# Kernel tuning notes

Measured on AMD Instinct MI355X. Metric: run time of the kernel, lower is better.

The kernel has to match this reference:

```python
import jax, jax.numpy as jnp
import numpy as np

N, F = 100000, 64   # input (up) nodes, feature dim
M, K = 100000, 32   # down nodes, neighbors per node


def setup_inputs() -> dict:
    key = jax.random.key(0)
    k1, k2, k3, k4 = jax.random.split(key, 4)
    features = jax.random.normal(k1, (N, F), dtype=jnp.float32)
    sel_idx_up = jax.random.randint(k2, (N, 1), 0, M, dtype=jnp.int64)
    weights_down = jax.random.uniform(k3, (M, K, 1), dtype=jnp.float32)
    nidx_down = jax.random.randint(k4, (M, K), 0, M, dtype=jnp.int64)
    return {
        "features": features,
        "weights_down": weights_down,
        "sel_idx_up": sel_idx_up,
        "nidx_down": nidx_down,
    }


def reference(features, weights_down, sel_idx_up, nidx_down):
    # PullDown, mode='mean', weights=None.
    m = weights_down.shape[0]
    f_dim = features.shape[1]
    # tf.scatter_nd: duplicate indices accumulate (add)
    down_f = jnp.zeros((m, f_dim), dtype=features.dtype).at[sel_idx_up[:, 0]].add(features)
    # acc_knn weighted mean over K neighbors; nidx == -1 means invalid (zero contribution)
    mask = nidx_down >= 0                              # [M, K]
    idx = jnp.where(mask, nidx_down, 0)
    gathered = down_f[idx] * weights_down              # [M, K, F]
    gathered = jnp.where(mask[..., None], gathered, jnp.zeros((), dtype=features.dtype))
    out = jnp.mean(gathered, axis=1)                   # divide by K, as acc_sum's *K implies
    return out.reshape(-1, f_dim)
```

## Files before the change

kernel.cpp:

```cpp
#include <hip/hip_runtime.h>
#include <hip/hip_bf16.h>

#define F_DIM 64
#define K_NB  32
#define CAP   16

typedef float        f32x4 __attribute__((ext_vector_type(4)));
typedef int          i32x4 __attribute__((ext_vector_type(4)));
typedef unsigned int u32;

__device__ inline u32 f2b(float f) {
    u32 u = __float_as_uint(f);
    u32 r = ((u >> 16) & 1u) + 0x7fffu;
    return (u + r) >> 16;
}
__device__ inline float blo(u32 u) { return __uint_as_float(u << 16); }
__device__ inline float bhi(u32 u) { return __uint_as_float(u & 0xffff0000u); }

__global__ __launch_bounds__(256) void bucket_fill_kernel(
    const int* __restrict__ sel_idx,
    int*       __restrict__ cnt,
    int*       __restrict__ bucket,
    int N)
{
    int i = blockIdx.x * blockDim.x + threadIdx.x;
    if (i >= N) return;
    int m = sel_idx[i];
    int slot = atomicAdd(&cnt[m], 1);
    if (slot < CAP) bucket[m * CAP + slot] = i;
}

__global__ __launch_bounds__(256) void build_down_f_bf16_kernel(
    const f32x4* __restrict__ features4,
    const int*   __restrict__ cnt,
    const int*   __restrict__ bucket,
    unsigned short* __restrict__ down_h,
    int M)
{
    int t = blockIdx.x * blockDim.x + threadIdx.x;
    int m = t >> 4;
    int q = t & 15;
    if (m >= M) return;
    int c = cnt[m]; c = c < CAP ? c : CAP;
    const int* bk = bucket + m * CAP;

    int b0 = bk[0], b1 = bk[1], b2 = bk[2], b3 = bk[3];
    int i0 = (0 < c) ? b0 : 0;  float g0 = (0 < c) ? 1.f : 0.f;
    int i1 = (1 < c) ? b1 : 0;  float g1 = (1 < c) ? 1.f : 0.f;
    int i2 = (2 < c) ? b2 : 0;  float g2 = (2 < c) ? 1.f : 0.f;
    int i3 = (3 < c) ? b3 : 0;  float g3 = (3 < c) ? 1.f : 0.f;

    f32x4 v0 = features4[(size_t)i0 * 16 + q];
    f32x4 v1 = features4[(size_t)i1 * 16 + q];
    f32x4 v2 = features4[(size_t)i2 * 16 + q];
    f32x4 v3 = features4[(size_t)i3 * 16 + q];

    f32x4 acc;
    acc.x = g0 * v0.x + g1 * v1.x + g2 * v2.x + g3 * v3.x;
    acc.y = g0 * v0.y + g1 * v1.y + g2 * v2.y + g3 * v3.y;
    acc.z = g0 * v0.z + g1 * v1.z + g2 * v2.z + g3 * v3.z;
    acc.w = g0 * v0.w + g1 * v1.w + g2 * v2.w + g3 * v3.w;

    if (c > 4) {
        for (int j = 4; j < c; ++j) {
            int i = bk[j];
            f32x4 v = features4[(size_t)i * 16 + q];
            acc.x += v.x; acc.y += v.y; acc.z += v.z; acc.w += v.w;
        }
    }
    uint2 o;
    o.x = f2b(acc.x) | (f2b(acc.y) << 16);
    o.y = f2b(acc.z) | (f2b(acc.w) << 16);
    *(uint2*)(down_h + (size_t)m * F_DIM + q * 4) = o;
}

__global__ __launch_bounds__(256) void gather_mean_bf16_kernel(
    const unsigned short* __restrict__ down_h,
    const f32x4*          __restrict__ weights4,
    const i32x4*          __restrict__ nidx4,
    f32x4*                __restrict__ out4,
    int M)
{
    int t = blockIdx.x * blockDim.x + threadIdx.x;
    int m = t >> 3;
    int q = t & 7;
    if (m >= M) return;

    const i32x4* ni = nidx4    + (size_t)m * (K_NB / 4);
    const f32x4* wp = weights4 + (size_t)m * (K_NB / 4);
    const uint4* base = (const uint4*)down_h + q;

    float a0 = 0.f, a1 = 0.f, a2 = 0.f, a3 = 0.f;
    float a4 = 0.f, a5 = 0.f, a6 = 0.f, a7 = 0.f;

    #pragma unroll
    for (int b = 0; b < 4; ++b) {
        i32x4 I0 = ni[2 * b], I1 = ni[2 * b + 1];
        f32x4 W0 = wp[2 * b], W1 = wp[2 * b + 1];
        int j0 = I0.x < 0 ? 0 : I0.x;  float w0 = I0.x < 0 ? 0.f : W0.x;
        int j1 = I0.y < 0 ? 0 : I0.y;  float w1 = I0.y < 0 ? 0.f : W0.y;
        int j2 = I0.z < 0 ? 0 : I0.z;  float w2 = I0.z < 0 ? 0.f : W0.z;
        int j3 = I0.w < 0 ? 0 : I0.w;  float w3 = I0.w < 0 ? 0.f : W0.w;
        int j4 = I1.x < 0 ? 0 : I1.x;  float w4 = I1.x < 0 ? 0.f : W1.x;
        int j5 = I1.y < 0 ? 0 : I1.y;  float w5 = I1.y < 0 ? 0.f : W1.y;
        int j6 = I1.z < 0 ? 0 : I1.z;  float w6 = I1.z < 0 ? 0.f : W1.z;
        int j7 = I1.w < 0 ? 0 : I1.w;  float w7 = I1.w < 0 ? 0.f : W1.w;

        uint4 g0 = base[(size_t)j0 * 8];
        uint4 g1 = base[(size_t)j1 * 8];
        uint4 g2 = base[(size_t)j2 * 8];
        uint4 g3 = base[(size_t)j3 * 8];
        uint4 g4 = base[(size_t)j4 * 8];
        uint4 g5 = base[(size_t)j5 * 8];
        uint4 g6 = base[(size_t)j6 * 8];
        uint4 g7 = base[(size_t)j7 * 8];

        a0 += w0 * blo(g0.x); a1 += w0 * bhi(g0.x); a2 += w0 * blo(g0.y); a3 += w0 * bhi(g0.y);
        a4 += w0 * blo(g0.z); a5 += w0 * bhi(g0.z); a6 += w0 * blo(g0.w); a7 += w0 * bhi(g0.w);
        a0 += w1 * blo(g1.x); a1 += w1 * bhi(g1.x); a2 += w1 * blo(g1.y); a3 += w1 * bhi(g1.y);
        a4 += w1 * blo(g1.z); a5 += w1 * bhi(g1.z); a6 += w1 * blo(g1.w); a7 += w1 * bhi(g1.w);
        a0 += w2 * blo(g2.x); a1 += w2 * bhi(g2.x); a2 += w2 * blo(g2.y); a3 += w2 * bhi(g2.y);
        a4 += w2 * blo(g2.z); a5 += w2 * bhi(g2.z); a6 += w2 * blo(g2.w); a7 += w2 * bhi(g2.w);
        a0 += w3 * blo(g3.x); a1 += w3 * bhi(g3.x); a2 += w3 * blo(g3.y); a3 += w3 * bhi(g3.y);
        a4 += w3 * blo(g3.z); a5 += w3 * bhi(g3.z); a6 += w3 * blo(g3.w); a7 += w3 * bhi(g3.w);
        a0 += w4 * blo(g4.x); a1 += w4 * bhi(g4.x); a2 += w4 * blo(g4.y); a3 += w4 * bhi(g4.y);
        a4 += w4 * blo(g4.z); a5 += w4 * bhi(g4.z); a6 += w4 * blo(g4.w); a7 += w4 * bhi(g4.w);
        a0 += w5 * blo(g5.x); a1 += w5 * bhi(g5.x); a2 += w5 * blo(g5.y); a3 += w5 * bhi(g5.y);
        a4 += w5 * blo(g5.z); a5 += w5 * bhi(g5.z); a6 += w5 * blo(g5.w); a7 += w5 * bhi(g5.w);
        a0 += w6 * blo(g6.x); a1 += w6 * bhi(g6.x); a2 += w6 * blo(g6.y); a3 += w6 * bhi(g6.y);
        a4 += w6 * blo(g6.z); a5 += w6 * bhi(g6.z); a6 += w6 * blo(g6.w); a7 += w6 * bhi(g6.w);
        a0 += w7 * blo(g7.x); a1 += w7 * bhi(g7.x); a2 += w7 * blo(g7.y); a3 += w7 * bhi(g7.y);
        a4 += w7 * blo(g7.z); a5 += w7 * bhi(g7.z); a6 += w7 * blo(g7.w); a7 += w7 * bhi(g7.w);
    }

    const float s = 1.0f / (float)K_NB;
    size_t o = (size_t)m * 16 + q * 2;
    f32x4 r0; r0.x = a0 * s; r0.y = a1 * s; r0.z = a2 * s; r0.w = a3 * s;
    f32x4 r1; r1.x = a4 * s; r1.y = a5 * s; r1.z = a6 * s; r1.w = a7 * s;
    out4[o + 0] = r0;
    out4[o + 1] = r1;
}

__global__ __launch_bounds__(256) void scatter_add_kernel(
    const float* __restrict__ features, const int* __restrict__ sel_idx,
    float* __restrict__ down_f, int N)
{
    int t = blockIdx.x * blockDim.x + threadIdx.x;
    int i  = t >> 5;
    int fp = (t & 31);
    if (i >= N) return;
    int dst = sel_idx[i];
    float2 v = ((const float2*)features)[(size_t)i * (F_DIM / 2) + fp];
    float* d = down_f + (size_t)dst * F_DIM + fp * 2;
    atomicAdd(d + 0, v.x);
    atomicAdd(d + 1, v.y);
}

__global__ __launch_bounds__(256) void gather_mean_f32_kernel(
    const float2* __restrict__ down_f2, const float* __restrict__ weights,
    const int* __restrict__ nidx, float2* __restrict__ out2, int M)
{
    int t  = blockIdx.x * blockDim.x + threadIdx.x;
    int m  = t >> 5;
    int fp = t & 31;
    if (m >= M) return;
    const i32x4* ni4 = (const i32x4*)(nidx    + (size_t)m * K_NB);
    const f32x4* wp4 = (const f32x4*)(weights + (size_t)m * K_NB);
    float accx = 0.f, accy = 0.f;
    #pragma unroll
    for (int q = 0; q < K_NB / 4; ++q) {
        i32x4 iv = ni4[q];
        f32x4 wv = wp4[q];
        int i0 = iv.x < 0 ? 0 : iv.x;  float w0 = iv.x < 0 ? 0.f : wv.x;
        int i1 = iv.y < 0 ? 0 : iv.y;  float w1 = iv.y < 0 ? 0.f : wv.y;
        int i2 = iv.z < 0 ? 0 : iv.z;  float w2 = iv.z < 0 ? 0.f : wv.z;
        int i3 = iv.w < 0 ? 0 : iv.w;  float w3 = iv.w < 0 ? 0.f : wv.w;
        float2 v0 = down_f2[(size_t)i0 * (F_DIM / 2) + fp];
        float2 v1 = down_f2[(size_t)i1 * (F_DIM / 2) + fp];
        float2 v2 = down_f2[(size_t)i2 * (F_DIM / 2) + fp];
        float2 v3 = down_f2[(size_t)i3 * (F_DIM / 2) + fp];
        accx += w0 * v0.x; accy += w0 * v0.y;
        accx += w1 * v1.x; accy += w1 * v1.y;
        accx += w2 * v2.x; accy += w2 * v2.y;
        accx += w3 * v3.x; accy += w3 * v3.y;
    }
    float2 r;
    r.x = accx * (1.0f / (float)K_NB);
    r.y = accy * (1.0f / (float)K_NB);
    out2[(size_t)m * (F_DIM / 2) + fp] = r;
}

extern "C" void kernel_launch(void* const* d_in, const int* in_sizes, int n_in,
                              void* d_out, int out_size, void* d_ws, size_t ws_size,
                              hipStream_t stream) {
    const float* features = (const float*)d_in[0];
    const float* weights  = (const float*)d_in[1];
    const int*   sel_idx  = (const int*)  d_in[2];
    const int*   nidx     = (const int*)  d_in[3];
    float*       out      = (float*)d_out;

    const int N = in_sizes[2];
    const int M = in_sizes[3] / K_NB;

    size_t downh_bytes  = (size_t)M * F_DIM * sizeof(unsigned short);
    size_t cnt_bytes    = (size_t)M * sizeof(int);
    size_t bucket_bytes = (size_t)M * CAP * sizeof(int);

    if (ws_size >= downh_bytes + cnt_bytes + bucket_bytes) {
        unsigned short* down_h = (unsigned short*)d_ws;
        int* cnt    = (int*)((char*)d_ws + downh_bytes);
        int* bucket = cnt + M;

        hipMemsetAsync(cnt, 0, cnt_bytes, stream);
        bucket_fill_kernel<<<(N + 255) / 256, 256, 0, stream>>>(
            sel_idx, cnt, bucket, N);
        build_down_f_bf16_kernel<<<(M * 16 + 255) / 256, 256, 0, stream>>>(
            (const f32x4*)features, cnt, bucket, down_h, M);
        gather_mean_bf16_kernel<<<(M * 8 + 255) / 256, 256, 0, stream>>>(
            down_h, (const f32x4*)weights, (const i32x4*)nidx,
            (f32x4*)out, M);
    } else {
        float* down_f = (float*)d_ws;
        hipMemsetAsync(down_f, 0, (size_t)M * F_DIM * sizeof(float), stream);
        scatter_add_kernel<<<(N * 32 + 255) / 256, 256, 0, stream>>>(
            features, sel_idx, down_f, N);
        gather_mean_f32_kernel<<<(M * 32 + 255) / 256, 256, 0, stream>>>(
            (const float2*)down_f, weights, nidx, (float2*)out, M);
    }
}
```

Before: 156.0 us.

## Fuse pulldown stages into one cooperative kernel with compacted bf16 table

Replaces the memset plus three kernel launches with a single cooperative persistent kernel that uses grid-wide syncs between the stages. Only occupied down nodes are stored, in a compacted bf16 table, and the neighbour indices are rewritten as packed 16-bit slot ids. Invalid or empty neighbours point to a zero row, so the per-neighbour mask selects are no longer needed. The aims are to cut launch overhead, shrink the gather working set to raise cache hits, and halve index traffic. The cost is four grid syncs and an extra remap pass, and the 16-bit packing only holds while the number of occupied nodes stays below 65536.

```diff
diff --git a/kernel.cpp b/kernel.cpp
--- a/kernel.cpp
+++ b/kernel.cpp
@@ -1,12 +1,18 @@
 #include <hip/hip_runtime.h>
-#include <hip/hip_bf16.h>
+#include <hip/hip_cooperative_groups.h>
+
+namespace cg = cooperative_groups;
 
 #define F_DIM 64
 #define K_NB  32
 #define CAP   16
+#define GRID_BLOCKS 1024
+#define BLOCK       256
 
 typedef float        f32x4 __attribute__((ext_vector_type(4)));
 typedef int          i32x4 __attribute__((ext_vector_type(4)));
+typedef unsigned int u32x4 __attribute__((ext_vector_type(4)));
+typedef unsigned int u32x2 __attribute__((ext_vector_type(2)));
 typedef unsigned int u32;
 
 __device__ inline u32 f2b(float f) {
@@ -16,6 +22,161 @@
 }
 __device__ inline float blo(u32 u) { return __uint_as_float(u << 16); }
 __device__ inline float bhi(u32 u) { return __uint_as_float(u & 0xffff0000u); }
+
+__global__ __launch_bounds__(BLOCK, 4) void fused_pulldown_kernel(
+    const f32x4* __restrict__ features4,
+    const f32x4* __restrict__ weights4,
+    const i32x4* __restrict__ nidx4,
+    const int*   __restrict__ sel_idx,
+    f32x4*       __restrict__ out4,
+    unsigned short* __restrict__ down_h,
+    int*         __restrict__ bucket,
+    int*         __restrict__ cnt,
+    int*         __restrict__ nz,
+    int*         __restrict__ remap,
+    int N, int M)
+{
+    cg::grid_group grid = cg::this_grid();
+    const int tid0    = blockIdx.x * BLOCK + threadIdx.x;
+    const int gstride = gridDim.x * blockDim.x;
+
+    for (int i = tid0; i < M; i += gstride) { cnt[i] = 0; remap[i] = 0; }
+    if (tid0 == 0) *nz = 0;
+    if (tid0 < 16) { u32x2 z; z.x = 0u; z.y = 0u; ((u32x2*)down_h)[tid0] = z; }
+    grid.sync();
+
+    for (int i = tid0; i < N; i += gstride) {
+        int m = sel_idx[i];
+        int slot = atomicAdd(&cnt[m], 1);
+        if (slot < CAP) bucket[m * CAP + slot] = i;
+        if (slot == 0) remap[m] = 1 + atomicAdd(nz, 1);
+    }
+    grid.sync();
+
+    for (int t = tid0; t < M * 16; t += gstride) {
+        int m = t >> 4;
+        int q = t & 15;
+        int c = cnt[m];
+        if (c == 0) continue;
+        c = c < CAP ? c : CAP;
+        int s = remap[m];
+        const i32x4* b4p = (const i32x4*)(bucket + m * CAP);
+        i32x4 b4 = b4p[0];
+
+        int i0 = b4.x;
+        int i1 = (1 < c) ? b4.y : 0;  float g1 = (1 < c) ? 1.f : 0.f;
+        int i2 = (2 < c) ? b4.z : 0;  float g2 = (2 < c) ? 1.f : 0.f;
+        int i3 = (3 < c) ? b4.w : 0;  float g3 = (3 < c) ? 1.f : 0.f;
+
+        f32x4 v0 = __builtin_nontemporal_load(&features4[(size_t)i0 * 16 + q]);
+        f32x4 v1 = __builtin_nontemporal_load(&features4[(size_t)i1 * 16 + q]);
+        f32x4 v2 = __builtin_nontemporal_load(&features4[(size_t)i2 * 16 + q]);
+        f32x4 v3 = __builtin_nontemporal_load(&features4[(size_t)i3 * 16 + q]);
+
+        f32x4 acc;
+        acc.x = v0.x + g1 * v1.x + g2 * v2.x + g3 * v3.x;
+        acc.y = v0.y + g1 * v1.y + g2 * v2.y + g3 * v3.y;
+        acc.z = v0.z + g1 * v1.z + g2 * v2.z + g3 * v3.z;
+        acc.w = v0.w + g1 * v1.w + g2 * v2.w + g3 * v3.w;
+
+        if (c > 4) {
+            const int* bk = bucket + m * CAP;
+            for (int j = 4; j < c; ++j) {
+                int i = bk[j];
+                f32x4 v = __builtin_nontemporal_load(&features4[(size_t)i * 16 + q]);
+                acc.x += v.x; acc.y += v.y; acc.z += v.z; acc.w += v.w;
+            }
+        }
+        u32x2 o;
+        o.x = f2b(acc.x) | (f2b(acc.y) << 16);
+        o.y = f2b(acc.z) | (f2b(acc.w) << 16);
+        *(u32x2*)(down_h + (size_t)s * F_DIM + q * 4) = o;
+    }
+    grid.sync();
+
+    {
+        u32x4* nidx_c = (u32x4*)bucket;
+        const int TT = M * (K_NB / 8);
+        for (int t = tid0; t < TT; t += gstride) {
+            i32x4 I0 = __builtin_nontemporal_load(nidx4 + 2 * t);
+            i32x4 I1 = __builtin_nontemporal_load(nidx4 + 2 * t + 1);
+            u32 r0 = (u32)remap[I0.x < 0 ? 0 : I0.x];  r0 = I0.x < 0 ? 0u : r0;
+            u32 r1 = (u32)remap[I0.y < 0 ? 0 : I0.y];  r1 = I0.y < 0 ? 0u : r1;
+            u32 r2 = (u32)remap[I0.z < 0 ? 0 : I0.z];  r2 = I0.z < 0 ? 0u : r2;
+            u32 r3 = (u32)remap[I0.w < 0 ? 0 : I0.w];  r3 = I0.w < 0 ? 0u : r3;
+            u32 r4 = (u32)remap[I1.x < 0 ? 0 : I1.x];  r4 = I1.x < 0 ? 0u : r4;
+            u32 r5 = (u32)remap[I1.y < 0 ? 0 : I1.y];  r5 = I1.y < 0 ? 0u : r5;
+            u32 r6 = (u32)remap[I1.z < 0 ? 0 : I1.z];  r6 = I1.z < 0 ? 0u : r6;
+            u32 r7 = (u32)remap[I1.w < 0 ? 0 : I1.w];  r7 = I1.w < 0 ? 0u : r7;
+            u32x4 o;
+            o.x = r0 | (r1 << 16);
+            o.y = r2 | (r3 << 16);
+            o.z = r4 | (r5 << 16);
+            o.w = r6 | (r7 << 16);
+            __builtin_nontemporal_store(o, nidx_c + t);
+        }
+    }
+    grid.sync();
+
+    {
+        const u32x4* nidx_c = (const u32x4*)bucket;
+        for (int t = tid0; t < M * 8; t += gstride) {
+            int m = t >> 3;
+            int q = t & 7;
+            const u32x4* ncp = nidx_c + (size_t)m * 4;
+            const f32x4* wp  = weights4 + (size_t)m * (K_NB / 4);
+            const unsigned char* bp =
+                (const unsigned char*)down_h + (unsigned)q * 16u;
+
+            float a0 = 0.f, a1 = 0.f, a2 = 0.f, a3 = 0.f;
+            float a4 = 0.f, a5 = 0.f, a6 = 0.f, a7 = 0.f;
+
+            #pragma unroll
+            for (int b = 0; b < 4; ++b) {
+                u32x4 I  = __builtin_nontemporal_load(ncp + b);
+                f32x4 W0 = __builtin_nontemporal_load(wp + 2 * b);
+                f32x4 W1 = __builtin_nontemporal_load(wp + 2 * b + 1);
+                u32 r0 = I.x & 0xffffu, r1 = I.x >> 16;
+                u32 r2 = I.y & 0xffffu, r3 = I.y >> 16;
+                u32 r4 = I.z & 0xffffu, r5 = I.z >> 16;
+                u32 r6 = I.w & 0xffffu, r7 = I.w >> 16;
+
+                u32x4 g0 = *(const u32x4*)(bp + (size_t)(r0 * 128u));
+                u32x4 g1 = *(const u32x4*)(bp + (size_t)(r1 * 128u));
+                u32x4 g2 = *(const u32x4*)(bp + (size_t)(r2 * 128u));
+                u32x4 g3 = *(const u32x4*)(bp + (size_t)(r3 * 128u));
+                u32x4 g4 = *(const u32x4*)(bp + (size_t)(r4 * 128u));
+                u32x4 g5 = *(const u32x4*)(bp + (size_t)(r5 * 128u));
+                u32x4 g6 = *(const u32x4*)(bp + (size_t)(r6 * 128u));
+                u32x4 g7 = *(const u32x4*)(bp + (size_t)(r7 * 128u));
+
+                a0 += W0.x * blo(g0.x); a1 += W0.x * bhi(g0.x); a2 += W0.x * blo(g0.y); a3 += W0.x * bhi(g0.y);
+                a4 += W0.x * blo(g0.z); a5 += W0.x * bhi(g0.z); a6 += W0.x * blo(g0.w); a7 += W0.x * bhi(g0.w);
+                a0 += W0.y * blo(g1.x); a1 += W0.y * bhi(g1.x); a2 += W0.y * blo(g1.y); a3 += W0.y * bhi(g1.y);
+                a4 += W0.y * blo(g1.z); a5 += W0.y * bhi(g1.z); a6 += W0.y * blo(g1.w); a7 += W0.y * bhi(g1.w);
+                a0 += W0.z * blo(g2.x); a1 += W0.z * bhi(g2.x); a2 += W0.z * blo(g2.y); a3 += W0.z * bhi(g2.y);
+                a4 += W0.z * blo(g2.z); a5 += W0.z * bhi(g2.z); a6 += W0.z * blo(g2.w); a7 += W0.z * bhi(g2.w);
+                a0 += W0.w * blo(g3.x); a1 += W0.w * bhi(g3.x); a2 += W0.w * blo(g3.y); a3 += W0.w * bhi(g3.y);
+                a4 += W0.w * blo(g3.z); a5 += W0.w * bhi(g3.z); a6 += W0.w * blo(g3.w); a7 += W0.w * bhi(g3.w);
+                a0 += W1.x * blo(g4.x); a1 += W1.x * bhi(g4.x); a2 += W1.x * blo(g4.y); a3 += W1.x * bhi(g4.y);
+                a4 += W1.x * blo(g4.z); a5 += W1.x * bhi(g4.z); a6 += W1.x * blo(g4.w); a7 += W1.x * bhi(g4.w);
+                a0 += W1.y * blo(g5.x); a1 += W1.y * bhi(g5.x); a2 += W1.y * blo(g5.y); a3 += W1.y * bhi(g5.y);
+                a4 += W1.y * blo(g5.z); a5 += W1.y * bhi(g5.z); a6 += W1.y * blo(g5.w); a7 += W1.y * bhi(g5.w);
+                a0 += W1.z * blo(g6.x); a1 += W1.z * bhi(g6.x); a2 += W1.z * blo(g6.y); a3 += W1.z * bhi(g6.y);
+                a4 += W1.z * blo(g6.z); a5 += W1.z * bhi(g6.z); a6 += W1.z * blo(g6.w); a7 += W1.z * bhi(g6.w);
+                a0 += W1.w * blo(g7.x); a1 += W1.w * bhi(g7.x); a2 += W1.w * blo(g7.y); a3 += W1.w * bhi(g7.y);
+                a4 += W1.w * blo(g7.z); a5 += W1.w * bhi(g7.z); a6 += W1.w * blo(g7.w); a7 += W1.w * bhi(g7.w);
+            }
+
+            const float s = 1.0f / (float)K_NB;
+            size_t o = (size_t)m * 16 + q * 2;
+            f32x4 r0v; r0v.x = a0 * s; r0v.y = a1 * s; r0v.z = a2 * s; r0v.w = a3 * s;
+            f32x4 r1v; r1v.x = a4 * s; r1v.y = a5 * s; r1v.z = a6 * s; r1v.w = a7 * s;
+            __builtin_nontemporal_store(r0v, &out4[o + 0]);
+            __builtin_nontemporal_store(r1v, &out4[o + 1]);
+        }
+    }
+}
 
 __global__ __launch_bounds__(256) void bucket_fill_kernel(
     const int* __restrict__ sel_idx,
@@ -68,10 +229,10 @@
             acc.x += v.x; acc.y += v.y; acc.z += v.z; acc.w += v.w;
         }
     }
-    uint2 o;
+    u32x2 o;
     o.x = f2b(acc.x) | (f2b(acc.y) << 16);
     o.y = f2b(acc.z) | (f2b(acc.w) << 16);
-    *(uint2*)(down_h + (size_t)m * F_DIM + q * 4) = o;
+    *(u32x2*)(down_h + (size_t)m * F_DIM + q * 4) = o;
 }
 
 __global__ __launch_bounds__(256) void gather_mean_bf16_kernel(
@@ -88,7 +249,7 @@
 
     const i32x4* ni = nidx4    + (size_t)m * (K_NB / 4);
     const f32x4* wp = weights4 + (size_t)m * (K_NB / 4);
-    const uint4* base = (const uint4*)down_h + q;
+    const u32x4* base = (const u32x4*)down_h + q;
 
     float a0 = 0.f, a1 = 0.f, a2 = 0.f, a3 = 0.f;
     float a4 = 0.f, a5 = 0.f, a6 = 0.f, a7 = 0.f;
@@ -106,14 +267,14 @@
         int j6 = I1.z < 0 ? 0 : I1.z;  float w6 = I1.z < 0 ? 0.f : W1.z;
         int j7 = I1.w < 0 ? 0 : I1.w;  float w7 = I1.w < 0 ? 0.f : W1.w;
 
-        uint4 g0 = base[(size_t)j0 * 8];
-        uint4 g1 = base[(size_t)j1 * 8];
-        uint4 g2 = base[(size_t)j2 * 8];
-        uint4 g3 = base[(size_t)j3 * 8];
-        uint4 g4 = base[(size_t)j4 * 8];
-        uint4 g5 = base[(size_t)j5 * 8];
-        uint4 g6 = base[(size_t)j6 * 8];
-        uint4 g7 = base[(size_t)j7 * 8];
+        u32x4 g0 = base[(size_t)j0 * 8];
+        u32x4 g1 = base[(size_t)j1 * 8];
+        u32x4 g2 = base[(size_t)j2 * 8];
+        u32x4 g3 = base[(size_t)j3 * 8];
+        u32x4 g4 = base[(size_t)j4 * 8];
+        u32x4 g5 = base[(size_t)j5 * 8];
+        u32x4 g6 = base[(size_t)j6 * 8];
+        u32x4 g7 = base[(size_t)j7 * 8];
 
         a0 += w0 * blo(g0.x); a1 += w0 * bhi(g0.x); a2 += w0 * blo(g0.y); a3 += w0 * bhi(g0.y);
         a4 += w0 * blo(g0.z); a5 += w0 * bhi(g0.z); a6 += w0 * blo(g0.w); a7 += w0 * bhi(g0.w);
@@ -202,26 +363,79 @@
     const int N = in_sizes[2];
     const int M = in_sizes[3] / K_NB;
 
-    size_t downh_bytes  = (size_t)M * F_DIM * sizeof(unsigned short);
+    size_t downh_bytes  = (size_t)(M + 1) * F_DIM * sizeof(unsigned short);
+    size_t bucket_bytes = (size_t)M * CAP * sizeof(int);
     size_t cnt_bytes    = (size_t)M * sizeof(int);
-    size_t bucket_bytes = (size_t)M * CAP * sizeof(int);
-
-    if (ws_size >= downh_bytes + cnt_bytes + bucket_bytes) {
+    size_t nz_bytes     = 16;
+    size_t remap_bytes  = (size_t)M * sizeof(int);
+
+    if (ws_size >= downh_bytes + bucket_bytes + cnt_bytes + nz_bytes + remap_bytes) {
         unsigned short* down_h = (unsigned short*)d_ws;
-        int* cnt    = (int*)((char*)d_ws + downh_bytes);
-        int* bucket = cnt + M;
-
-        hipMemsetAsync(cnt, 0, cnt_bytes, stream);
-        bucket_fill_kernel<<<(N + 255) / 256, 256, 0, stream>>>(
-            sel_idx, cnt, bucket, N);
-        build_down_f_bf16_kernel<<<(M * 16 + 255) / 256, 256, 0, stream>>>(
-            (const f32x4*)features, cnt, bucket, down_h, M);
-        gather_mean_bf16_kernel<<<(M * 8 + 255) / 256, 256, 0, stream>>>(
-            down_h, (const f32x4*)weights, (const i32x4*)nidx,
-            (f32x4*)out, M);
+        int* bucket = (int*)((char*)d_ws + downh_bytes);
+        int* cnt    = (int*)((char*)d_ws + downh_bytes + bucket_bytes);
+        int* nz     = (int*)((char*)cnt + cnt_bytes);
+        int* remap  = (int*)((char*)nz + nz_bytes);
+
+        static int coop_state = 0;
+        static int coop_grid  = 0;
+        if (coop_state == 0 && coop_grid == 0) {
+            int maxB = 0, cus = 0, dev = 0;
+            (void)hipGetDevice(&dev);
+            if (hipOccupancyMaxActiveBlocksPerMultiprocessor(
+                    &maxB, (const void*)fused_pulldown_kernel, BLOCK, 0) == hipSuccess &&
+                hipDeviceGetAttribute(&cus, hipDeviceAttributeMultiprocessorCount,
+                                      dev) == hipSuccess &&
+                maxB > 0 && cus > 0) {
+                long cap = (long)maxB * (long)cus;
+                coop_grid = (int)(cap < GRID_BLOCKS ? cap : GRID_BLOCKS);
+            } else {
+                coop_state = -1;
+                coop_grid  = -1;
+            }
+        }
+
+        hipStreamCaptureStatus cap_st = hipStreamCaptureStatusNone;
+        (void)hipStreamIsCapturing(stream, &cap_st);
+        bool capturing = (cap_st != hipStreamCaptureStatusNone);
+        bool try_coop = (coop_state == 1) || (coop_state == 0 && !capturing);
+
+        bool done = false;
+        if (try_coop && coop_grid > 0) {
+            const f32x4* features4 = (const f32x4*)features;
+            const f32x4* weights4  = (const f32x4*)weights;
+            const i32x4* nidx4     = (const i32x4*)nidx;
+            f32x4*       out4      = (f32x4*)out;
+            int Nv = N, Mv = M;
+            void* args[] = {
+                (void*)&features4, (void*)&weights4, (void*)&nidx4,
+                (void*)&sel_idx,   (void*)&out4,     (void*)&down_h,
+                (void*)&bucket,    (void*)&cnt,      (void*)&nz,
+                (void*)&remap,     (void*)&Nv,       (void*)&Mv,
+            };
+            hipError_t err = hipLaunchCooperativeKernel(
+                (void*)fused_pulldown_kernel, dim3(coop_grid), dim3(BLOCK),
+                args, 0, stream);
+            if (err == hipSuccess) {
+                done = true;
+                if (coop_state == 0) coop_state = 1;
+            } else {
+                coop_state = -1;
+            }
+        }
+
+        if (!done) {
+            (void)hipMemsetAsync(cnt, 0, cnt_bytes, stream);
+            bucket_fill_kernel<<<(N + 255) / 256, 256, 0, stream>>>(
+                sel_idx, cnt, bucket, N);
+            build_down_f_bf16_kernel<<<(M * 16 + 255) / 256, 256, 0, stream>>>(
+                (const f32x4*)features, cnt, bucket, down_h, M);
+            gather_mean_bf16_kernel<<<(M * 8 + 255) / 256, 256, 0, stream>>>(
+                down_h, (const f32x4*)weights, (const i32x4*)nidx,
+                (f32x4*)out, M);
+        }
     } else {
         float* down_f = (float*)d_ws;
-        hipMemsetAsync(down_f, 0, (size_t)M * F_DIM * sizeof(float), stream);
+        (void)hipMemsetAsync(down_f, 0, (size_t)M * F_DIM * sizeof(float), stream);
         scatter_add_kernel<<<(N * 32 + 255) / 256, 256, 0, stream>>>(
             features, sel_idx, down_f, N);
         gather_mean_f32_kernel<<<(M * 32 + 255) / 256, 256, 0, stream>>>(
```

After: 436.2 us. 2.8x slower.

## Fuse three pulldown kernels into one persistent kernel with grid barriers

Applied to the files above, without the earlier changes.

Replaces the bucket-fill, bf16 build, and gather-mean launches with a single persistent grid-stride kernel. Stages are separated by software grid barriers built on atomic counters and flags kept in the workspace. The aim is to remove per-launch overhead and inter-kernel gaps. In exchange, the grid is capped by occupancy, spin-barriers add cost, and correctness relies on all blocks being co-resident.

```diff
diff --git a/kernel.cpp b/kernel.cpp
--- a/kernel.cpp
+++ b/kernel.cpp
@@ -1,12 +1,15 @@
 #include <hip/hip_runtime.h>
-#include <hip/hip_bf16.h>
 
 #define F_DIM 64
 #define K_NB  32
 #define CAP   16
+#define BLOCK 256
+#define MAX_GRID 2048
 
 typedef float        f32x4 __attribute__((ext_vector_type(4)));
 typedef int          i32x4 __attribute__((ext_vector_type(4)));
+typedef unsigned int u32x4 __attribute__((ext_vector_type(4)));
+typedef unsigned int u32x2 __attribute__((ext_vector_type(2)));
 typedef unsigned int u32;
 
 __device__ inline u32 f2b(float f) {
@@ -17,11 +20,149 @@
 __device__ inline float blo(u32 u) { return __uint_as_float(u << 16); }
 __device__ inline float bhi(u32 u) { return __uint_as_float(u & 0xffff0000u); }
 
+__device__ inline void grid_barrier(int* state, int idx, int nblocks) {
+    __syncthreads();
+    if (threadIdx.x == 0) {
+        int* arrive = state + idx * 64;
+        int* flag   = state + idx * 64 + 32;
+        __threadfence();
+        int prev = __hip_atomic_fetch_add(arrive, 1, __ATOMIC_ACQ_REL,
+                                          __HIP_MEMORY_SCOPE_AGENT);
+        if (prev == nblocks - 1) {
+            __hip_atomic_store(flag, 1, __ATOMIC_RELEASE,
+                               __HIP_MEMORY_SCOPE_AGENT);
+        } else {
+            while (__hip_atomic_load(flag, __ATOMIC_ACQUIRE,
+                                     __HIP_MEMORY_SCOPE_AGENT) == 0) {
+                __builtin_amdgcn_s_sleep(8);
+            }
+        }
+        __threadfence();
+    }
+    __syncthreads();
+}
+
+__global__ __launch_bounds__(BLOCK) void fused_pulldown_kernel(
+    const f32x4* __restrict__ features4,
+    const f32x4* __restrict__ weights4,
+    const i32x4* __restrict__ nidx4,
+    const int*   __restrict__ sel_idx,
+    f32x4*       __restrict__ out4,
+    unsigned short* __restrict__ down_h,
+    int*         __restrict__ bucket,
+    int*         __restrict__ cnt,
+    int*         __restrict__ bstate,
+    int N, int M, int nblocks)
+{
+    const int tid0    = blockIdx.x * BLOCK + threadIdx.x;
+    const int gstride = gridDim.x * BLOCK;
+
+    for (int i = tid0; i < N; i += gstride) {
+        int m = sel_idx[i];
+        int slot = atomicAdd(&cnt[m], 1);
+        if (slot < CAP) bucket[m * CAP + slot] = i;
+    }
+    grid_barrier(bstate, 0, nblocks);
+
+    for (int t = tid0; t < M * 16; t += gstride) {
+        int m = t >> 4;
+        int q = t & 15;
+        int c = cnt[m]; c = c < CAP ? c : CAP;
+        i32x4 b4 = *(const i32x4*)(bucket + m * CAP);
+
+        int i0 = (0 < c) ? b4.x : 0;  float g0 = (0 < c) ? 1.f : 0.f;
+        int i1 = (1 < c) ? b4.y : 0;  float g1 = (1 < c) ? 1.f : 0.f;
+        int i2 = (2 < c) ? b4.z : 0;  float g2 = (2 < c) ? 1.f : 0.f;
+        int i3 = (3 < c) ? b4.w : 0;  float g3 = (3 < c) ? 1.f : 0.f;
+
+        f32x4 v0 = features4[(size_t)i0 * 16 + q];
+        f32x4 v1 = features4[(size_t)i1 * 16 + q];
+        f32x4 v2 = features4[(size_t)i2 * 16 + q];
+        f32x4 v3 = features4[(size_t)i3 * 16 + q];
+
+        f32x4 acc;
+        acc.x = g0 * v0.x + g1 * v1.x + g2 * v2.x + g3 * v3.x;
+        acc.y = g0 * v0.y + g1 * v1.y + g2 * v2.y + g3 * v3.y;
+        acc.z = g0 * v0.z + g1 * v1.z + g2 * v2.z + g3 * v3.z;
+        acc.w = g0 * v0.w + g1 * v1.w + g2 * v2.w + g3 * v3.w;
+
+        if (c > 4) {
+            const int* bk = bucket + m * CAP;
+            for (int j = 4; j < c; ++j) {
+                int i = bk[j];
+                f32x4 v = features4[(size_t)i * 16 + q];
+                acc.x += v.x; acc.y += v.y; acc.z += v.z; acc.w += v.w;
+            }
+        }
+        u32x2 o;
+        o.x = f2b(acc.x) | (f2b(acc.y) << 16);
+        o.y = f2b(acc.z) | (f2b(acc.w) << 16);
+        *(u32x2*)(down_h + (size_t)m * F_DIM + q * 4) = o;
+    }
+    grid_barrier(bstate, 1, nblocks);
+
+    for (int t = tid0; t < M * 8; t += gstride) {
+        int m = t >> 3;
+        int q = t & 7;
+        const i32x4* ni = nidx4    + (size_t)m * (K_NB / 4);
+        const f32x4* wp = weights4 + (size_t)m * (K_NB / 4);
+        const u32x4* base = (const u32x4*)down_h + q;
+
+        float a0 = 0.f, a1 = 0.f, a2 = 0.f, a3 = 0.f;
+        float a4 = 0.f, a5 = 0.f, a6 = 0.f, a7 = 0.f;
+
+        #pragma unroll
+        for (int b = 0; b < 4; ++b) {
+            i32x4 I0 = ni[2 * b], I1 = ni[2 * b + 1];
+            f32x4 W0 = wp[2 * b], W1 = wp[2 * b + 1];
+            int j0 = I0.x < 0 ? 0 : I0.x;  float w0 = I0.x < 0 ? 0.f : W0.x;
+            int j1 = I0.y < 0 ? 0 : I0.y;  float w1 = I0.y < 0 ? 0.f : W0.y;
+            int j2 = I0.z < 0 ? 0 : I0.z;  float w2 = I0.z < 0 ? 0.f : W0.z;
+            int j3 = I0.w < 0 ? 0 : I0.w;  float w3 = I0.w < 0 ? 0.f : W0.w;
+            int j4 = I1.x < 0 ? 0 : I1.x;  float w4 = I1.x < 0 ? 0.f : W1.x;
+            int j5 = I1.y < 0 ? 0 : I1.y;  float w5 = I1.y < 0 ? 0.f : W1.y;
+            int j6 = I1.z < 0 ? 0 : I1.z;  float w6 = I1.z < 0 ? 0.f : W1.z;
+            int j7 = I1.w < 0 ? 0 : I1.w;  float w7 = I1.w < 0 ? 0.f : W1.w;
+
+            u32x4 g0 = base[(size_t)j0 * 8];
+            u32x4 g1 = base[(size_t)j1 * 8];
+            u32x4 g2 = base[(size_t)j2 * 8];
+            u32x4 g3 = base[(size_t)j3 * 8];
+            u32x4 g4 = base[(size_t)j4 * 8];
+            u32x4 g5 = base[(size_t)j5 * 8];
+            u32x4 g6 = base[(size_t)j6 * 8];
+            u32x4 g7 = base[(size_t)j7 * 8];
+
+            a0 += w0 * blo(g0.x); a1 += w0 * bhi(g0.x); a2 += w0 * blo(g0.y); a3 += w0 * bhi(g0.y);
+            a4 += w0 * blo(g0.z); a5 += w0 * bhi(g0.z); a6 += w0 * blo(g0.w); a7 += w0 * bhi(g0.w);
+            a0 += w1 * blo(g1.x); a1 += w1 * bhi(g1.x); a2 += w1 * blo(g1.y); a3 += w1 * bhi(g1.y);
+            a4 += w1 * blo(g1.z); a5 += w1 * bhi(g1.z); a6 += w1 * blo(g1.w); a7 += w1 * bhi(g1.w);
+            a0 += w2 * blo(g2.x); a1 += w2 * bhi(g2.x); a2 += w2 * blo(g2.y); a3 += w2 * bhi(g2.y);
+            a4 += w2 * blo(g2.z); a5 += w2 * bhi(g2.z); a6 += w2 * blo(g2.w); a7 += w2 * bhi(g2.w);
+            a0 += w3 * blo(g3.x); a1 += w3 * bhi(g3.x); a2 += w3 * blo(g3.y); a3 += w3 * bhi(g3.y);
+            a4 += w3 * blo(g3.z); a5 += w3 * bhi(g3.z); a6 += w3 * blo(g3.w); a7 += w3 * bhi(g3.w);
+            a0 += w4 * blo(g4.x); a1 += w4 * bhi(g4.x); a2 += w4 * blo(g4.y); a3 += w4 * bhi(g4.y);
+            a4 += w4 * blo(g4.z); a5 += w4 * bhi(g4.z); a6 += w4 * blo(g4.w); a7 += w4 * bhi(g4.w);
+            a0 += w5 * blo(g5.x); a1 += w5 * bhi(g5.x); a2 += w5 * blo(g5.y); a3 += w5 * bhi(g5.y);
+            a4 += w5 * blo(g5.z); a5 += w5 * bhi(g5.z); a6 += w5 * blo(g5.w); a7 += w5 * bhi(g5.w);
+            a0 += w6 * blo(g6.x); a1 += w6 * bhi(g6.x); a2 += w6 * blo(g6.y); a3 += w6 * bhi(g6.y);
+            a4 += w6 * blo(g6.z); a5 += w6 * bhi(g6.z); a6 += w6 * blo(g6.w); a7 += w6 * bhi(g6.w);
+            a0 += w7 * blo(g7.x); a1 += w7 * bhi(g7.x); a2 += w7 * blo(g7.y); a3 += w7 * bhi(g7.y);
+            a4 += w7 * blo(g7.z); a5 += w7 * bhi(g7.z); a6 += w7 * blo(g7.w); a7 += w7 * bhi(g7.w);
+        }
+
+        const float s = 1.0f / (float)K_NB;
+        size_t o = (size_t)m * 16 + q * 2;
+        f32x4 r0; r0.x = a0 * s; r0.y = a1 * s; r0.z = a2 * s; r0.w = a3 * s;
+        f32x4 r1; r1.x = a4 * s; r1.y = a5 * s; r1.z = a6 * s; r1.w = a7 * s;
+        out4[o + 0] = r0;
+        out4[o + 1] = r1;
+    }
+}
+
 __global__ __launch_bounds__(256) void bucket_fill_kernel(
-    const int* __restrict__ sel_idx,
-    int*       __restrict__ cnt,
-    int*       __restrict__ bucket,
-    int N)
+    const int* __restrict__ sel_idx, int* __restrict__ cnt,
+    int* __restrict__ bucket, int N)
 {
     int i = blockIdx.x * blockDim.x + threadIdx.x;
     if (i >= N) return;
@@ -31,11 +172,8 @@
 }
 
 __global__ __launch_bounds__(256) void build_down_f_bf16_kernel(
-    const f32x4* __restrict__ features4,
-    const int*   __restrict__ cnt,
-    const int*   __restrict__ bucket,
-    unsigned short* __restrict__ down_h,
-    int M)
+    const f32x4* __restrict__ features4, const int* __restrict__ cnt,
+    const int* __restrict__ bucket, unsigned short* __restrict__ down_h, int M)
 {
     int t = blockIdx.x * blockDim.x + threadIdx.x;
     int m = t >> 4;
@@ -68,18 +206,16 @@
             acc.x += v.x; acc.y += v.y; acc.z += v.z; acc.w += v.w;
         }
     }
-    uint2 o;
+    u32x2 o;
     o.x = f2b(acc.x) | (f2b(acc.y) << 16);
     o.y = f2b(acc.z) | (f2b(acc.w) << 16);
-    *(uint2*)(down_h + (size_t)m * F_DIM + q * 4) = o;
+    *(u32x2*)(down_h + (size_t)m * F_DIM + q * 4) = o;
 }
 
 __global__ __launch_bounds__(256) void gather_mean_bf16_kernel(
     const unsigned short* __restrict__ down_h,
-    const f32x4*          __restrict__ weights4,
-    const i32x4*          __restrict__ nidx4,
-    f32x4*                __restrict__ out4,
-    int M)
+    const f32x4* __restrict__ weights4, const i32x4* __restrict__ nidx4,
+    f32x4* __restrict__ out4, int M)
 {
     int t = blockIdx.x * blockDim.x + threadIdx.x;
     int m = t >> 3;
@@ -88,7 +224,7 @@
 
     const i32x4* ni = nidx4    + (size_t)m * (K_NB / 4);
     const f32x4* wp = weights4 + (size_t)m * (K_NB / 4);
-    const uint4* base = (const uint4*)down_h + q;
+    const u32x4* base = (const u32x4*)down_h + q;
 
     float a0 = 0.f, a1 = 0.f, a2 = 0.f, a3 = 0.f;
     float a4 = 0.f, a5 = 0.f, a6 = 0.f, a7 = 0.f;
@@ -106,14 +242,14 @@
         int j6 = I1.z < 0 ? 0 : I1.z;  float w6 = I1.z < 0 ? 0.f : W1.z;
         int j7 = I1.w < 0 ? 0 : I1.w;  float w7 = I1.w < 0 ? 0.f : W1.w;
 
-        uint4 g0 = base[(size_t)j0 * 8];
-        uint4 g1 = base[(size_t)j1 * 8];
-        uint4 g2 = base[(size_t)j2 * 8];
-        uint4 g3 = base[(size_t)j3 * 8];
-        uint4 g4 = base[(size_t)j4 * 8];
-        uint4 g5 = base[(size_t)j5 * 8];
-        uint4 g6 = base[(size_t)j6 * 8];
-        uint4 g7 = base[(size_t)j7 * 8];
+        u32x4 g0 = base[(size_t)j0 * 8];
+        u32x4 g1 = base[(size_t)j1 * 8];
+        u32x4 g2 = base[(size_t)j2 * 8];
+        u32x4 g3 = base[(size_t)j3 * 8];
+        u32x4 g4 = base[(size_t)j4 * 8];
+        u32x4 g5 = base[(size_t)j5 * 8];
+        u32x4 g6 = base[(size_t)j6 * 8];
+        u32x4 g7 = base[(size_t)j7 * 8];
 
         a0 += w0 * blo(g0.x); a1 += w0 * bhi(g0.x); a2 += w0 * blo(g0.y); a3 += w0 * bhi(g0.y);
         a4 += w0 * blo(g0.z); a5 += w0 * bhi(g0.z); a6 += w0 * blo(g0.w); a7 += w0 * bhi(g0.w);
@@ -203,25 +339,53 @@
     const int M = in_sizes[3] / K_NB;
 
     size_t downh_bytes  = (size_t)M * F_DIM * sizeof(unsigned short);
+    size_t bucket_bytes = (size_t)M * CAP * sizeof(int);
     size_t cnt_bytes    = (size_t)M * sizeof(int);
-    size_t bucket_bytes = (size_t)M * CAP * sizeof(int);
-
-    if (ws_size >= downh_bytes + cnt_bytes + bucket_bytes) {
+    size_t bstate_bytes = 512;
+
+    if (ws_size >= downh_bytes + bucket_bytes + cnt_bytes + bstate_bytes) {
         unsigned short* down_h = (unsigned short*)d_ws;
-        int* cnt    = (int*)((char*)d_ws + downh_bytes);
-        int* bucket = cnt + M;
-
-        hipMemsetAsync(cnt, 0, cnt_bytes, stream);
-        bucket_fill_kernel<<<(N + 255) / 256, 256, 0, stream>>>(
-            sel_idx, cnt, bucket, N);
-        build_down_f_bf16_kernel<<<(M * 16 + 255) / 256, 256, 0, stream>>>(
-            (const f32x4*)features, cnt, bucket, down_h, M);
-        gather_mean_bf16_kernel<<<(M * 8 + 255) / 256, 256, 0, stream>>>(
-            down_h, (const f32x4*)weights, (const i32x4*)nidx,
-            (f32x4*)out, M);
+        int* bucket = (int*)((char*)d_ws + downh_bytes);
+        int* cnt    = (int*)((char*)d_ws + downh_bytes + bucket_bytes);
+        int* bstate = cnt + M;
+
+        static int fused_grid = 0;
+        if (fused_grid == 0) {
+            int maxB = 0, cus = 0, dev = 0;
+            (void)hipGetDevice(&dev);
+            if (hipOccupancyMaxActiveBlocksPerMultiprocessor(
+                    &maxB, (const void*)fused_pulldown_kernel, BLOCK, 0) == hipSuccess &&
+                hipDeviceGetAttribute(&cus, hipDeviceAttributeMultiprocessorCount,
+                                      dev) == hipSuccess &&
+                maxB > 0 && cus > 0) {
+                int per_cu = (maxB > 1) ? (maxB - 1) : 1;
+                long g = (long)per_cu * (long)cus;
+                if (g > MAX_GRID) g = MAX_GRID;
+                fused_grid = (int)g;
+            } else {
+                fused_grid = -1;
+            }
+        }
+
+        if (fused_grid > 0) {
+            (void)hipMemsetAsync(cnt, 0, cnt_bytes + bstate_bytes, stream);
+            fused_pulldown_kernel<<<fused_grid, BLOCK, 0, stream>>>(
+                (const f32x4*)features, (const f32x4*)weights,
+                (const i32x4*)nidx, sel_idx, (f32x4*)out,
+                down_h, bucket, cnt, bstate, N, M, fused_grid);
+        } else {
+            (void)hipMemsetAsync(cnt, 0, cnt_bytes, stream);
+            bucket_fill_kernel<<<(N + 255) / 256, 256, 0, stream>>>(
+                sel_idx, cnt, bucket, N);
+            build_down_f_bf16_kernel<<<(M * 16 + 255) / 256, 256, 0, stream>>>(
+                (const f32x4*)features, cnt, bucket, down_h, M);
+            gather_mean_bf16_kernel<<<(M * 8 + 255) / 256, 256, 0, stream>>>(
+                down_h, (const f32x4*)weights, (const i32x4*)nidx,
+                (f32x4*)out, M);
+        }
     } else {
         float* down_f = (float*)d_ws;
-        hipMemsetAsync(down_f, 0, (size_t)M * F_DIM * sizeof(float), stream);
+        (void)hipMemsetAsync(down_f, 0, (size_t)M * F_DIM * sizeof(float), stream);
         scatter_add_kernel<<<(N * 32 + 255) / 256, 256, 0, stream>>>(
             features, sel_idx, down_f, N);
         gather_mean_f32_kernel<<<(M * 32 + 255) / 256, 256, 0, stream>>>(
```

Measured after the change: 228.7 us. +46.6%, slower.
